# Performance work log

Measured on AMD Instinct MI355X. Metric: run time of the kernel, lower is better.

The kernel has to match this reference:

```python
import jax, jax.numpy as jnp
import numpy as np

NUM_HEADS = 8
LATENT_FRAME = 4
D_MODEL = 1024
D_FF = 1024  # dim_feedforward == output_dim in the torch module
N_LAYERS = 6
IN_DIM = 128
LN_EPS = 1e-5


def get_slopes(n):
    # standard ALiBi slopes for power-of-two head counts: 2^{-8(i+1)/n}
    return jnp.asarray([2.0 ** (-8.0 * (i + 1) / n) for i in range(n)], jnp.float32)


def alibi_mask(num_heads, T):
    # non-causal ('future') ALiBi: additive bias -slope_h * |i - j|, shape (H, T, T)
    dist = jnp.abs(jnp.arange(T)[:, None] - jnp.arange(T)[None, :]).astype(jnp.float32)
    return -get_slopes(num_heads)[:, None, None] * dist


def layernorm(x, g, b):
    m = jnp.mean(x, axis=-1, keepdims=True)
    v = jnp.mean((x - m) ** 2, axis=-1, keepdims=True)
    return (x - m) * jax.lax.rsqrt(v + LN_EPS) * g + b


def encoder_layer(x, p, mask):
    # torch TransformerEncoderLayer, post-norm, gelu(exact), dropout=0
    B, T, D = x.shape
    H, Dh = NUM_HEADS, D // NUM_HEADS
    qkv = x @ p['in_w'].T + p['in_b']                      # (B,T,3D)
    q, k, v = jnp.split(qkv, 3, axis=-1)
    hsplit = lambda t: t.reshape(B, T, H, Dh).transpose(0, 2, 1, 3)  # (B,H,T,Dh)
    q, k, v = hsplit(q), hsplit(k), hsplit(v)
    scores = jnp.einsum('bhqd,bhkd->bhqk', q, k) / float(np.sqrt(Dh)) + mask[None]
    attn = jax.nn.softmax(scores, axis=-1)
    o = jnp.einsum('bhqk,bhkd->bhqd', attn, v).transpose(0, 2, 1, 3).reshape(B, T, D)
    o = o @ p['out_w'].T + p['out_b']
    x = layernorm(x + o, p['ln1_g'], p['ln1_b'])
    ff = jax.nn.gelu(x @ p['ff1_w'].T + p['ff1_b'], approximate=False) @ p['ff2_w'].T + p['ff2_b']
    return layernorm(x + ff, p['ln2_g'], p['ln2_b'])


def setup_inputs() -> dict:
    key = jax.random.key(0)
    ks = iter(jax.random.split(key, 32))
    s = 0.02
    B, T, F = 8, 2048, IN_DIM
    Fs = F * LATENT_FRAME  # 512
    inp = {
        'x': jax.random.normal(next(ks), (B, T, F), jnp.float32),
        'pre_w': jax.random.normal(next(ks), (D_MODEL, Fs), jnp.float32) * s,
        'pre_b': jnp.zeros((D_MODEL,), jnp.float32),
        'in_w': jax.random.normal(next(ks), (N_LAYERS, 3 * D_MODEL, D_MODEL), jnp.float32) * s,
        'in_b': jnp.zeros((N_LAYERS, 3 * D_MODEL), jnp.float32),
        'out_w': jax.random.normal(next(ks), (N_LAYERS, D_MODEL, D_MODEL), jnp.float32) * s,
        'out_b': jnp.zeros((N_LAYERS, D_MODEL), jnp.float32),
        'ln1_g': jnp.ones((N_LAYERS, D_MODEL), jnp.float32),
        'ln1_b': jnp.zeros((N_LAYERS, D_MODEL), jnp.float32),
        'ff1_w': jax.random.normal(next(ks), (N_LAYERS, D_FF, D_MODEL), jnp.float32) * s,
        'ff1_b': jnp.zeros((N_LAYERS, D_FF), jnp.float32),
        'ff2_w': jax.random.normal(next(ks), (N_LAYERS, D_MODEL, D_FF), jnp.float32) * s,
        'ff2_b': jnp.zeros((N_LAYERS, D_MODEL), jnp.float32),
        'ln2_g': jnp.ones((N_LAYERS, D_MODEL), jnp.float32),
        'ln2_b': jnp.zeros((N_LAYERS, D_MODEL), jnp.float32),
        'post_w': jax.random.normal(next(ks), (D_MODEL, D_MODEL), jnp.float32) * s,
        'post_b': jnp.zeros((D_MODEL,), jnp.float32),
    }
    return inp


def reference(x, pre_w, pre_b, in_w, in_b, out_w, out_b, ln1_g, ln1_b,
              ff1_w, ff1_b, ff2_w, ff2_b, ln2_g, ln2_b, post_w, post_b):
    B, T, F = x.shape
    Tl = T // LATENT_FRAME
    x = x.reshape(B, Tl, F * LATENT_FRAME)
    x = x @ pre_w.T + pre_b                     # (B, Tl, D)
    mask = alibi_mask(NUM_HEADS, Tl)            # (H, Tl, Tl), shared by all batches
    layers = dict(in_w=in_w, in_b=in_b, out_w=out_w, out_b=out_b,
                  ln1_g=ln1_g, ln1_b=ln1_b, ff1_w=ff1_w, ff1_b=ff1_b,
                  ff2_w=ff2_w, ff2_b=ff2_b, ln2_g=ln2_g, ln2_b=ln2_b)
    def step(h, p):
        return encoder_layer(h, p, mask), None
    x, _ = jax.lax.scan(step, x, layers)
    return x @ post_w.T + post_b
```

## Files before the change

### kernel.cpp

```cpp
#include <hip/hip_runtime.h>
#include <hip/hip_bf16.h>

#define B 8
#define TL 512
#define M_ROWS 4096
#define D 1024
#define DFF 1024
#define H 8
#define DH 128
#define NL 6

typedef unsigned short ushort_t;
typedef unsigned int uint_t;
typedef short bf16x8 __attribute__((ext_vector_type(8)));
typedef float f32x4 __attribute__((ext_vector_type(4)));

__device__ __forceinline__ ushort_t f2bf(float f) {
    uint_t u = __float_as_uint(f);
    u += 0x7FFFu + ((u >> 16) & 1u);
    return (ushort_t)(u >> 16);
}
__device__ __forceinline__ float gelu_exact(float x) {
    return 0.5f * x * (1.0f + erff(x * 0.70710678118654752f));
}
__device__ __forceinline__ void gload_lds16(const ushort_t* g, ushort_t* l) {
    __builtin_amdgcn_global_load_lds(
        (const __attribute__((address_space(1))) void*)g,
        (__attribute__((address_space(3))) void*)l, 16, 0, 0);
}

struct CvtArgs {
    const float* s[7];
    ushort_t* d[7];
    int nq[7];
    int bstart[8];
};

__global__ __launch_bounds__(256) void cvt_all(CvtArgs a) {
    const int bid = blockIdx.x;
#pragma unroll
    for (int seg = 0; seg < 7; ++seg) {
        const int b0 = a.bstart[seg], b1 = a.bstart[seg + 1];
        if (bid < b0 || bid >= b1) continue;
        const int stride = (b1 - b0) * 256;
        const float* s = a.s[seg];
        ushort_t* d = a.d[seg];
        const int nq = a.nq[seg];
        for (int i = (bid - b0) * 256 + threadIdx.x; i < nq; i += stride) {
            float4 v = *(const float4*)(s + (size_t)i * 4);
            ushort4 o;
            o.x = f2bf(v.x); o.y = f2bf(v.y); o.z = f2bf(v.z); o.w = f2bf(v.w);
            *(ushort4*)(d + (size_t)i * 4) = o;
        }
    }
}

#define LSLOT64(r, c) (((r) * 8 + ((c) ^ ((r) & 7))) * 8)

__global__ __launch_bounds__(512) void gemm_n128(
    const ushort_t* __restrict__ A, const ushort_t* __restrict__ W,
    const float* __restrict__ bias, float* __restrict__ Cf,
    ushort_t* __restrict__ Cb, int M, int N, int K, int do_gelu) {
    extern __shared__ ushort_t lds[];

    const int tid = threadIdx.x;
    const int lane = tid & 63;
    const int w = tid >> 6;
    const int wm = w >> 2;
    const int wn = w & 3;
    const int bm = blockIdx.y * 128;
    const int bn = blockIdx.x * 128;
    const int fr = lane & 15;
    const int fq = lane >> 4;

    const ushort_t* gA[2];
    const ushort_t* gB[2];
    int sdst[2];
#pragma unroll
    for (int u = 0; u < 2; ++u) {
        int s = tid + u * 512;
        int r = s >> 3, c = (s & 7) ^ (r & 7);
        gA[u] = A + (size_t)(bm + r) * K + c * 8;
        gB[u] = W + (size_t)(bn + r) * K + c * 8;
        sdst[u] = s * 8;
    }

    int aoff[4][2], boff[2][2];
#pragma unroll
    for (int ti = 0; ti < 4; ++ti)
#pragma unroll
        for (int ks = 0; ks < 2; ++ks)
            aoff[ti][ks] = LSLOT64(wm * 64 + ti * 16 + fr, ks * 4 + fq);
#pragma unroll
    for (int tj = 0; tj < 2; ++tj)
#pragma unroll
        for (int ks = 0; ks < 2; ++ks)
            boff[tj][ks] = LSLOT64(wn * 32 + tj * 16 + fr, ks * 4 + fq);

    f32x4 acc[4][2];
#pragma unroll
    for (int i = 0; i < 4; ++i)
#pragma unroll
        for (int j = 0; j < 2; ++j) acc[i][j] = (f32x4){0.f, 0.f, 0.f, 0.f};

    auto stage = [&](int buf, int k0) {
#pragma unroll
        for (int u = 0; u < 2; ++u)
            gload_lds16(gA[u] + k0, &lds[buf * 8192 + sdst[u]]);
#pragma unroll
        for (int u = 0; u < 2; ++u)
            gload_lds16(gB[u] + k0, &lds[16384 + buf * 8192 + sdst[u]]);
    };
    auto comp = [&](int buf) {
#pragma unroll
        for (int ks = 0; ks < 2; ++ks) {
            bf16x8 af[4], bfv[2];
#pragma unroll
            for (int ti = 0; ti < 4; ++ti)
                af[ti] = *(const bf16x8*)&lds[buf * 8192 + aoff[ti][ks]];
#pragma unroll
            for (int tj = 0; tj < 2; ++tj)
                bfv[tj] = *(const bf16x8*)&lds[16384 + buf * 8192 + boff[tj][ks]];
#pragma unroll
            for (int i = 0; i < 4; ++i)
#pragma unroll
                for (int j = 0; j < 2; ++j)
                    acc[i][j] = __builtin_amdgcn_mfma_f32_16x16x32_bf16(
                        af[i], bfv[j], acc[i][j], 0, 0, 0);
        }
    };

    const int NT = K >> 6;
    stage(0, 0);
    __syncthreads();
    int buf = 0;
    for (int t = 0; t < NT; ++t) {
        if (t + 1 < NT) stage(buf ^ 1, (t + 1) * 64);
        comp(buf);
        __syncthreads();
        buf ^= 1;
    }

    float bv[2];
#pragma unroll
    for (int tj = 0; tj < 2; ++tj) bv[tj] = bias[bn + wn * 32 + tj * 16 + fr];

    float* eps = (float*)lds;
#pragma unroll
    for (int p = 0; p < 2; ++p) {
        if (p) __syncthreads();
        if (wm == p) {
#pragma unroll
            for (int ti = 0; ti < 4; ++ti)
#pragma unroll
                for (int tj = 0; tj < 2; ++tj)
#pragma unroll
                    for (int r = 0; r < 4; ++r) {
                        float v = acc[ti][tj][r] + bv[tj];
                        if (do_gelu) v = gelu_exact(v);
                        eps[(ti * 16 + fq * 4 + r) * 132 +
                            wn * 32 + tj * 16 + fr] = v;
                    }
        }
        __syncthreads();
#pragma unroll
        for (int k = 0; k < 4; ++k) {
            int f = tid + k * 512;
            int row = f >> 5, c4 = f & 31;
            float4 v = *(const float4*)&eps[row * 132 + c4 * 4];
            const size_t off = (size_t)(bm + p * 64 + row) * N + bn + c4 * 4;
            if (Cf) *(float4*)(Cf + off) = v;
            if (Cb) {
                ushort4 ob;
                ob.x = f2bf(v.x); ob.y = f2bf(v.y);
                ob.z = f2bf(v.z); ob.w = f2bf(v.w);
                *(ushort4*)(Cb + off) = ob;
            }
        }
    }
}

#define QPHASE(par, mh, nh, LOADA, ...)                                        \
    {                                                                          \
        if (LOADA) {                                                           \
            _Pragma("unroll") for (int im = 0; im < 4; ++im)                   \
                _Pragma("unroll") for (int ks = 0; ks < 2; ++ks)               \
                    af[im][ks] = *(const bf16x8*)&AsB[(par)*16384 +            \
                                                     (mh)*8192 + aoff[im][ks]];\
        }                                                                      \
        _Pragma("unroll") for (int jn = 0; jn < 2; ++jn)                       \
            _Pragma("unroll") for (int ks = 0; ks < 2; ++ks)                   \
                bfv[jn][ks] = *(const bf16x8*)&BsB[(par)*16384 +               \
                                                  (nh)*8192 + boff[jn][ks]];   \
        __VA_ARGS__;                                                           \
        __builtin_amdgcn_s_barrier();                                          \
        asm volatile("s_waitcnt lgkmcnt(0)" ::: "memory");                     \
        __builtin_amdgcn_sched_barrier(0);                                     \
        __builtin_amdgcn_s_setprio(1);                                         \
        _Pragma("unroll") for (int im = 0; im < 4; ++im)                       \
            _Pragma("unroll") for (int jn = 0; jn < 2; ++jn)                   \
                _Pragma("unroll") for (int ks = 0; ks < 2; ++ks)               \
                    acc[(mh)*4 + im][(nh)*2 + jn] =                            \
                        __builtin_amdgcn_mfma_f32_16x16x32_bf16(               \
                            af[im][ks], bfv[jn][ks],                           \
                            acc[(mh)*4 + im][(nh)*2 + jn], 0, 0, 0);           \
        __builtin_amdgcn_s_setprio(0);                                         \
        asm volatile("s_waitcnt vmcnt(4)" ::: "memory");                       \
        __builtin_amdgcn_s_barrier();                                          \
    }

__global__ __launch_bounds__(512, 2) void gemm_qkv256(
    const ushort_t* __restrict__ A, const ushort_t* __restrict__ W,
    const float* __restrict__ bias, ushort_t* __restrict__ Qb,
    ushort_t* __restrict__ Kb, ushort_t* __restrict__ Vt) {
    extern __shared__ ushort_t lds[];
    ushort_t* AsB = lds;
    ushort_t* BsB = lds + 32768;
    const int K = 1024;

    const int bid = blockIdx.x;
    const int wg = (bid & 7) * 24 + (bid >> 3);
    const int by = wg / 12, bx = wg - by * 12;
    const int bm = by * 256, bn = bx * 256;

    const int tid = threadIdx.x;
    const int lane = tid & 63;
    const int w = tid >> 6;
    const int wm = w >> 2;
    const int wn = w & 3;
    const int fr = lane & 15;
    const int fq = lane >> 4;

    const ushort_t* gA[2];
    const ushort_t* gB[2];
    int sdst[2];
#pragma unroll
    for (int u = 0; u < 2; ++u) {
        int s = tid + u * 512;
        int r = s >> 3, c = (s & 7) ^ (r & 7);
        gA[u] = A + (size_t)(bm + r) * K + c * 8;
        gB[u] = W + (size_t)(bn + r) * K + c * 8;
        sdst[u] = s * 8;
    }

    int aoff[4][2], boff[2][2];
#pragma unroll
    for (int im = 0; im < 4; ++im)
#pragma unroll
        for (int ks = 0; ks < 2; ++ks)
            aoff[im][ks] = LSLOT64(wm * 64 + im * 16 + fr, ks * 4 + fq);
#pragma unroll
    for (int jn = 0; jn < 2; ++jn)
#pragma unroll
        for (int ks = 0; ks < 2; ++ks)
            boff[jn][ks] = LSLOT64(wn * 32 + jn * 16 + fr, ks * 4 + fq);

    f32x4 acc[8][4];
#pragma unroll
    for (int i = 0; i < 8; ++i)
#pragma unroll
        for (int j = 0; j < 4; ++j) acc[i][j] = (f32x4){0.f, 0.f, 0.f, 0.f};

    auto stageA = [&](int p, int h, int tk) {
#pragma unroll
        for (int u = 0; u < 2; ++u)
            gload_lds16(gA[u] + (size_t)h * 128 * K + tk * 64,
                        &AsB[p * 16384 + h * 8192 + sdst[u]]);
    };
    auto stageB = [&](int p, int h, int tk) {
#pragma unroll
        for (int u = 0; u < 2; ++u)
            gload_lds16(gB[u] + (size_t)h * 128 * K + tk * 64,
                        &BsB[p * 16384 + h * 8192 + sdst[u]]);
    };

    stageA(0, 0, 0); stageB(0, 0, 0); stageB(0, 1, 0); stageA(0, 1, 0);
    asm volatile("s_waitcnt vmcnt(0)" ::: "memory");
    __builtin_amdgcn_s_barrier();

    bf16x8 af[4][2], bfv[2][2];

#pragma unroll 1
    for (int it = 0; it < 8; ++it) {
        const int t0 = 2 * it;
        QPHASE(0, 0, 0, 1, { stageA(1, 0, t0 + 1); })
        QPHASE(0, 0, 1, 0, { stageB(1, 0, t0 + 1); })
        QPHASE(0, 1, 0, 1, { stageB(1, 1, t0 + 1); })
        QPHASE(0, 1, 1, 0, { stageA(1, 1, t0 + 1); })
        const bool st = (it < 7);
        QPHASE(1, 0, 0, 1, { if (st) stageA(0, 0, t0 + 2); })
        QPHASE(1, 0, 1, 0, { if (st) stageB(0, 0, t0 + 2); })
        QPHASE(1, 1, 0, 1, { if (st) stageB(0, 1, t0 + 2); })
        QPHASE(1, 1, 1, 0, { if (st) stageA(0, 1, t0 + 2); })
    }

    const float qscale = 0.08838834764831845f;
#pragma unroll
    for (int j = 0; j < 4; ++j) {
        const int n = bn + (j >> 1) * 128 + wn * 32 + (j & 1) * 16 + fr;
        const float bv = bias[n];
#pragma unroll
        for (int i = 0; i < 8; ++i) {
            const int m0 = bm + (i >> 2) * 128 + wm * 64 + (i & 3) * 16 + fq * 4;
            f32x4 a = acc[i][j];
            if (n < D) {
#pragma unroll
                for (int r = 0; r < 4; ++r)
                    Qb[(size_t)(m0 + r) * D + n] = f2bf((a[r] + bv) * qscale);
            } else if (n < 2 * D) {
#pragma unroll
                for (int r = 0; r < 4; ++r)
                    Kb[(size_t)(m0 + r) * D + (n - D)] = f2bf(a[r] + bv);
            } else {
                const int h = (n - 2 * D) >> 7;
                const int dh = (n - 2 * D) & 127;
                const int bb = m0 >> 9;
                const int t = m0 & 511;
                ushort4 pk;
                pk.x = f2bf(a[0] + bv); pk.y = f2bf(a[1] + bv);
                pk.z = f2bf(a[2] + bv); pk.w = f2bf(a[3] + bv);
                *(ushort4*)&Vt[((size_t)(bb * H + h) * DH + dh) * TL + t] = pk;
            }
        }
    }
}

#define LSW16(r, g) ((((r) << 4) + ((g) ^ ((r) & 7))) << 3)
#define LSW8(r, g) ((((r) << 3) + ((g) ^ ((r) & 7))) << 3)

__global__ __launch_bounds__(256, 2) void attn_mfma(
    const ushort_t* __restrict__ Qb, const ushort_t* __restrict__ Kb,
    const ushort_t* __restrict__ Vt, ushort_t* __restrict__ Ab) {
    __shared__ ushort_t Qs[64 * 128];
    __shared__ ushort_t Ks[64 * 128];
    __shared__ ushort_t Vts[128 * 64];
    __shared__ ushort_t Ps[64 * 72];

    const int q0 = blockIdx.x * 64;
    const int bh = blockIdx.y;
    const int b = bh >> 3;
    const int h = bh & 7;
    const int tid = threadIdx.x;
    const int lane = tid & 63;
    const int w = tid >> 6;
    const int fr = lane & 15;
    const int fq = lane >> 4;

    const float slope = exp2f(-(float)(h + 1));

#pragma unroll
    for (int kk = 0; kk < 4; ++kk) {
        int s = tid + kk * 256;
        int r = s >> 4, gp = s & 15, gl = gp ^ (r & 7);
        gload_lds16(Qb + (size_t)(b * TL + q0 + r) * D + h * DH + gl * 8,
                    &Qs[s * 8]);
    }

    f32x4 o8[8];
    float m_i[4], l_i[4];
#pragma unroll
    for (int nt = 0; nt < 8; ++nt) o8[nt] = (f32x4){0.f, 0.f, 0.f, 0.f};
#pragma unroll
    for (int r = 0; r < 4; ++r) { m_i[r] = -1e30f; l_i[r] = 0.f; }

    for (int kt = 0; kt < TL / 64; ++kt) {
        __syncthreads();
#pragma unroll
        for (int kk = 0; kk < 4; ++kk) {
            int s = tid + kk * 256;
            int r = s >> 4, gp = s & 15, gl = gp ^ (r & 7);
            gload_lds16(Kb + (size_t)(b * TL + kt * 64 + r) * D + h * DH + gl * 8,
                        &Ks[s * 8]);
        }
#pragma unroll
        for (int kk = 0; kk < 4; ++kk) {
            int s = tid + kk * 256;
            int r = s >> 3, gp = s & 7, gl = gp ^ (r & 7);
            gload_lds16(Vt + ((size_t)bh * DH + r) * TL + kt * 64 + gl * 8,
                        &Vts[s * 8]);
        }
        __syncthreads();

        f32x4 sacc[4];
#pragma unroll
        for (int jt = 0; jt < 4; ++jt) sacc[jt] = (f32x4){0.f, 0.f, 0.f, 0.f};
        __builtin_amdgcn_s_setprio(1);
#pragma unroll
        for (int s4 = 0; s4 < 4; ++s4) {
            bf16x8 aq = *(const bf16x8*)&Qs[LSW16(w * 16 + fr, s4 * 4 + fq)];
#pragma unroll
            for (int jt = 0; jt < 4; ++jt) {
                bf16x8 kb = *(const bf16x8*)&Ks[LSW16(jt * 16 + fr, s4 * 4 + fq)];
                sacc[jt] = __builtin_amdgcn_mfma_f32_16x16x32_bf16(
                    aq, kb, sacc[jt], 0, 0, 0);
            }
        }
        __builtin_amdgcn_s_setprio(0);

        const int iq = q0 + w * 16 + fq * 4;
        const int jk = kt * 64 + fr;
        float al[4];
#pragma unroll
        for (int r = 0; r < 4; ++r) {
            float sv[4];
#pragma unroll
            for (int jt = 0; jt < 4; ++jt)
                sv[jt] = sacc[jt][r] -
                         slope * fabsf((float)(iq + r - jk - jt * 16));
            float mx = fmaxf(fmaxf(sv[0], sv[1]), fmaxf(sv[2], sv[3]));
            mx = fmaxf(mx, __shfl_xor(mx, 1));
            mx = fmaxf(mx, __shfl_xor(mx, 2));
            mx = fmaxf(mx, __shfl_xor(mx, 4));
            mx = fmaxf(mx, __shfl_xor(mx, 8));
            float mnew = fmaxf(m_i[r], mx);
            al[r] = __expf(m_i[r] - mnew);
            float rs = 0.f;
#pragma unroll
            for (int jt = 0; jt < 4; ++jt) {
                sv[jt] = __expf(sv[jt] - mnew);
                rs += sv[jt];
            }
            rs += __shfl_xor(rs, 1);
            rs += __shfl_xor(rs, 2);
            rs += __shfl_xor(rs, 4);
            rs += __shfl_xor(rs, 8);
            l_i[r] = l_i[r] * al[r] + rs;
            m_i[r] = mnew;
            const int prow = w * 16 + fq * 4 + r;
#pragma unroll
            for (int jt = 0; jt < 4; ++jt)
                Ps[prow * 72 + jt * 16 + fr] = f2bf(sv[jt]);
        }
#pragma unroll
        for (int nt = 0; nt < 8; ++nt)
#pragma unroll
            for (int r = 0; r < 4; ++r) o8[nt][r] *= al[r];

        __builtin_amdgcn_s_setprio(1);
#pragma unroll
        for (int s2 = 0; s2 < 2; ++s2) {
            bf16x8 pa = *(const bf16x8*)&Ps[(w * 16 + fr) * 72 + s2 * 32 + fq * 8];
#pragma unroll
            for (int nt = 0; nt < 8; ++nt) {
                bf16x8 vb = *(const bf16x8*)&Vts[LSW8(nt * 16 + fr, s2 * 4 + fq)];
                o8[nt] = __builtin_amdgcn_mfma_f32_16x16x32_bf16(
                    pa, vb, o8[nt], 0, 0, 0);
            }
        }
        __builtin_amdgcn_s_setprio(0);
    }

#pragma unroll
    for (int r = 0; r < 4; ++r) {
        float inv = 1.f / l_i[r];
        const size_t base = (size_t)(b * TL + q0 + w * 16 + fq * 4 + r) * D + h * DH;
#pragma unroll
        for (int nt = 0; nt < 8; ++nt)
            Ab[base + nt * 16 + fr] = f2bf(o8[nt][r] * inv);
    }
}

__global__ __launch_bounds__(256) void add_ln(const float* __restrict__ x,
                                              const float* __restrict__ y,
                                              const float* __restrict__ g,
                                              const float* __restrict__ bta,
                                              float* __restrict__ out,
                                              ushort_t* __restrict__ outb) {
    const int row = blockIdx.x * 4 + (threadIdx.x >> 6);
    const int lane = threadIdx.x & 63;
    const size_t rbase = (size_t)row * D;

    float4 v[4];
#pragma unroll
    for (int j = 0; j < 4; ++j) {
        float4 xv = *(const float4*)(x + rbase + lane * 4 + j * 256);
        float4 yv = *(const float4*)(y + rbase + lane * 4 + j * 256);
        v[j].x = xv.x + yv.x; v[j].y = xv.y + yv.y;
        v[j].z = xv.z + yv.z; v[j].w = xv.w + yv.w;
    }

    float s = 0.f;
#pragma unroll
    for (int j = 0; j < 4; ++j) s += v[j].x + v[j].y + v[j].z + v[j].w;
#pragma unroll
    for (int off = 32; off; off >>= 1) s += __shfl_xor(s, off);
    const float mean = s * (1.f / (float)D);

    float sq = 0.f;
#pragma unroll
    for (int j = 0; j < 4; ++j) {
        float d0 = v[j].x - mean, d1 = v[j].y - mean;
        float d2 = v[j].z - mean, d3 = v[j].w - mean;
        sq += d0 * d0 + d1 * d1 + d2 * d2 + d3 * d3;
    }
#pragma unroll
    for (int off = 32; off; off >>= 1) sq += __shfl_xor(sq, off);
    const float var = sq * (1.f / (float)D);
    const float inv = rsqrtf(var + 1e-5f);

#pragma unroll
    for (int j = 0; j < 4; ++j) {
        const int col = lane * 4 + j * 256;
        float4 gv = *(const float4*)(g + col);
        float4 bv = *(const float4*)(bta + col);
        float4 o;
        o.x = (v[j].x - mean) * inv * gv.x + bv.x;
        o.y = (v[j].y - mean) * inv * gv.y + bv.y;
        o.z = (v[j].z - mean) * inv * gv.z + bv.z;
        o.w = (v[j].w - mean) * inv * gv.w + bv.w;
        *(float4*)(out + rbase + col) = o;
        ushort4 ob;
        ob.x = f2bf(o.x); ob.y = f2bf(o.y); ob.z = f2bf(o.z); ob.w = f2bf(o.w);
        *(ushort4*)(outb + rbase + col) = ob;
    }
}

extern "C" void kernel_launch(void* const* d_in, const int* in_sizes, int n_in,
                              void* d_out, int out_size, void* d_ws, size_t ws_size,
                              hipStream_t stream) {
    const float* x_in   = (const float*)d_in[0];
    const float* pre_w  = (const float*)d_in[1];
    const float* pre_b  = (const float*)d_in[2];
    const float* in_w   = (const float*)d_in[3];
    const float* in_b   = (const float*)d_in[4];
    const float* out_w  = (const float*)d_in[5];
    const float* out_b  = (const float*)d_in[6];
    const float* ln1_g  = (const float*)d_in[7];
    const float* ln1_b  = (const float*)d_in[8];
    const float* ff1_w  = (const float*)d_in[9];
    const float* ff1_b  = (const float*)d_in[10];
    const float* ff2_w  = (const float*)d_in[11];
    const float* ff2_b  = (const float*)d_in[12];
    const float* ln2_g  = (const float*)d_in[13];
    const float* ln2_b  = (const float*)d_in[14];
    const float* post_w = (const float*)d_in[15];
    const float* post_b = (const float*)d_in[16];

    static bool attr_set = false;
    if (!attr_set) {
        hipFuncSetAttribute((const void*)gemm_qkv256,
                            hipFuncAttributeMaxDynamicSharedMemorySize, 131072);
        hipFuncSetAttribute((const void*)gemm_n128,
                            hipFuncAttributeMaxDynamicSharedMemorySize, 65536);
        attr_set = true;
    }

    float* X = (float*)d_ws;
    float* Y = X + (size_t)M_ROWS * D;
    ushort_t* Xb   = (ushort_t*)(Y + (size_t)M_ROWS * D);
    ushort_t* Ab   = Xb + (size_t)M_ROWS * D;
    ushort_t* Qb   = Ab + (size_t)M_ROWS * D;
    ushort_t* Kb   = Qb + (size_t)M_ROWS * D;
    ushort_t* Vt   = Kb + (size_t)M_ROWS * D;
    ushort_t* xinb = Vt + (size_t)M_ROWS * D;
    ushort_t* pwb  = xinb + (size_t)M_ROWS * 512;
    ushort_t* iwb  = pwb + (size_t)D * 512;
    ushort_t* owb  = iwb + (size_t)NL * 3 * D * D;
    ushort_t* f1wb = owb + (size_t)NL * D * D;
    ushort_t* f2wb = f1wb + (size_t)NL * DFF * D;
    ushort_t* powb = f2wb + (size_t)NL * D * DFF;

    const dim3 blk(256);

    CvtArgs ca;
    ca.s[0] = x_in;   ca.d[0] = xinb; ca.nq[0] = (M_ROWS * 512) / 4;
    ca.s[1] = pre_w;  ca.d[1] = pwb;  ca.nq[1] = (D * 512) / 4;
    ca.s[2] = in_w;   ca.d[2] = iwb;  ca.nq[2] = (NL * 3 * D * D) / 4;
    ca.s[3] = out_w;  ca.d[3] = owb;  ca.nq[3] = (NL * D * D) / 4;
    ca.s[4] = ff1_w;  ca.d[4] = f1wb; ca.nq[4] = (NL * DFF * D) / 4;
    ca.s[5] = ff2_w;  ca.d[5] = f2wb; ca.nq[5] = (NL * D * DFF) / 4;
    ca.s[6] = post_w; ca.d[6] = powb; ca.nq[6] = (D * D) / 4;
    {
        long long total = 0;
        for (int i = 0; i < 7; ++i) total += ca.nq[i];
        long long cum = 0;
        ca.bstart[0] = 0;
        for (int i = 0; i < 7; ++i) {
            cum += ca.nq[i];
            ca.bstart[i + 1] = (int)((cum * 4096) / total);
        }
        ca.bstart[7] = 4096;
    }
    cvt_all<<<4096, blk, 0, stream>>>(ca);

    const dim3 gN128(D / 128, M_ROWS / 128);

    gemm_n128<<<gN128, dim3(512), 65536, stream>>>(xinb, pwb, pre_b, X, Xb,
                                                   M_ROWS, D, 512, 0);

    for (int l = 0; l < NL; ++l) {
        gemm_qkv256<<<dim3(192), dim3(512), 131072, stream>>>(
            Xb, iwb + (size_t)l * 3 * D * D, in_b + (size_t)l * 3 * D,
            Qb, Kb, Vt);
        attn_mfma<<<dim3(TL / 64, B * H), blk, 0, stream>>>(Qb, Kb, Vt, Ab);
        gemm_n128<<<gN128, dim3(512), 65536, stream>>>(
            Ab, owb + (size_t)l * D * D, out_b + (size_t)l * D, Y, nullptr,
            M_ROWS, D, D, 0);
        add_ln<<<dim3(M_ROWS / 4), blk, 0, stream>>>(X, Y, ln1_g + (size_t)l * D,
                                                     ln1_b + (size_t)l * D, X, Xb);
        gemm_n128<<<gN128, dim3(512), 65536, stream>>>(
            Xb, f1wb + (size_t)l * DFF * D, ff1_b + (size_t)l * DFF, nullptr, Ab,
            M_ROWS, DFF, D, 1);
        gemm_n128<<<gN128, dim3(512), 65536, stream>>>(
            Ab, f2wb + (size_t)l * D * DFF, ff2_b + (size_t)l * D, Y, nullptr,
            M_ROWS, D, DFF, 0);
        add_ln<<<dim3(M_ROWS / 4), blk, 0, stream>>>(X, Y, ln2_g + (size_t)l * D,
                                                     ln2_b + (size_t)l * D, X, Xb);
    }

    gemm_n128<<<gN128, dim3(512), 65536, stream>>>(Xb, powb, post_b,
                                                   (float*)d_out, nullptr,
                                                   M_ROWS, D, D, 0);
}
```

Baseline: 1.127 ms.

## Use triple-buffered K pipeline in GEMMs and replace 256-tile QKV kernel with 128-tile

Replaces the double-buffered K loop in gemm_n128 with a three-stage LDS ring buffer that keeps two tiles in flight, using vmcnt waits and one barrier per step, and raises MFMA priority during compute. The hand-scheduled 256x256 QKV GEMM is swapped for a 128x128 variant that uses the same pipeline, with 768 blocks instead of 192, and stages Q/K output through LDS for coalesced stores. The intent is to hide global load latency and improve occupancy and load balance. In exchange it uses more LDS per block (96KB), which may cut blocks per CU, and it loses the 256-tile data reuse in QKV.

```diff
diff --git a/kernel.cpp b/kernel.cpp
--- a/kernel.cpp
+++ b/kernel.cpp
@@ -57,6 +57,26 @@
 
 #define LSLOT64(r, c) (((r) * 8 + ((c) ^ ((r) & 7))) * 8)
 
+#define PIPE_K_LOOP(NT)                                                        \
+    {                                                                          \
+        stage(0, 0);                                                           \
+        stage(1, 64);                                                          \
+        int bsel = 0;                                                          \
+        for (int t = 0; t < (NT)-1; ++t) {                                     \
+            asm volatile("s_waitcnt vmcnt(4)" ::: "memory");                   \
+            __builtin_amdgcn_s_barrier();                                      \
+            comp(bsel);                                                        \
+            if (t + 2 < (NT)) {                                                \
+                int nb = bsel + 2; if (nb >= 3) nb -= 3;                       \
+                stage(nb, (t + 2) * 64);                                       \
+            }                                                                  \
+            ++bsel; if (bsel == 3) bsel = 0;                                   \
+        }                                                                      \
+        asm volatile("s_waitcnt vmcnt(0)" ::: "memory");                       \
+        __builtin_amdgcn_s_barrier();                                          \
+        comp(bsel);                                                            \
+    }
+
 __global__ __launch_bounds__(512) void gemm_n128(
     const ushort_t* __restrict__ A, const ushort_t* __restrict__ W,
     const float* __restrict__ bias, float* __restrict__ Cf,
@@ -106,10 +126,10 @@
     auto stage = [&](int buf, int k0) {
 #pragma unroll
         for (int u = 0; u < 2; ++u)
-            gload_lds16(gA[u] + k0, &lds[buf * 8192 + sdst[u]]);
+            gload_lds16(gA[u] + k0, &lds[buf * 16384 + sdst[u]]);
 #pragma unroll
         for (int u = 0; u < 2; ++u)
-            gload_lds16(gB[u] + k0, &lds[16384 + buf * 8192 + sdst[u]]);
+            gload_lds16(gB[u] + k0, &lds[buf * 16384 + 8192 + sdst[u]]);
     };
     auto comp = [&](int buf) {
 #pragma unroll
@@ -117,29 +137,24 @@
             bf16x8 af[4], bfv[2];
 #pragma unroll
             for (int ti = 0; ti < 4; ++ti)
-                af[ti] = *(const bf16x8*)&lds[buf * 8192 + aoff[ti][ks]];
+                af[ti] = *(const bf16x8*)&lds[buf * 16384 + aoff[ti][ks]];
 #pragma unroll
             for (int tj = 0; tj < 2; ++tj)
-                bfv[tj] = *(const bf16x8*)&lds[16384 + buf * 8192 + boff[tj][ks]];
+                bfv[tj] = *(const bf16x8*)&lds[buf * 16384 + 8192 + boff[tj][ks]];
+            __builtin_amdgcn_s_setprio(1);
 #pragma unroll
             for (int i = 0; i < 4; ++i)
 #pragma unroll
                 for (int j = 0; j < 2; ++j)
                     acc[i][j] = __builtin_amdgcn_mfma_f32_16x16x32_bf16(
                         af[i], bfv[j], acc[i][j], 0, 0, 0);
+            __builtin_amdgcn_s_setprio(0);
         }
     };
 
     const int NT = K >> 6;
-    stage(0, 0);
+    PIPE_K_LOOP(NT)
     __syncthreads();
-    int buf = 0;
-    for (int t = 0; t < NT; ++t) {
-        if (t + 1 < NT) stage(buf ^ 1, (t + 1) * 64);
-        comp(buf);
-        __syncthreads();
-        buf ^= 1;
-    }
 
     float bv[2];
 #pragma unroll
@@ -180,48 +195,17 @@
     }
 }
 
-#define QPHASE(par, mh, nh, LOADA, ...)                                        \
-    {                                                                          \
-        if (LOADA) {                                                           \
-            _Pragma("unroll") for (int im = 0; im < 4; ++im)                   \
-                _Pragma("unroll") for (int ks = 0; ks < 2; ++ks)               \
-                    af[im][ks] = *(const bf16x8*)&AsB[(par)*16384 +            \
-                                                     (mh)*8192 + aoff[im][ks]];\
-        }                                                                      \
-        _Pragma("unroll") for (int jn = 0; jn < 2; ++jn)                       \
-            _Pragma("unroll") for (int ks = 0; ks < 2; ++ks)                   \
-                bfv[jn][ks] = *(const bf16x8*)&BsB[(par)*16384 +               \
-                                                  (nh)*8192 + boff[jn][ks]];   \
-        __VA_ARGS__;                                                           \
-        __builtin_amdgcn_s_barrier();                                          \
-        asm volatile("s_waitcnt lgkmcnt(0)" ::: "memory");                     \
-        __builtin_amdgcn_sched_barrier(0);                                     \
-        __builtin_amdgcn_s_setprio(1);                                         \
-        _Pragma("unroll") for (int im = 0; im < 4; ++im)                       \
-            _Pragma("unroll") for (int jn = 0; jn < 2; ++jn)                   \
-                _Pragma("unroll") for (int ks = 0; ks < 2; ++ks)               \
-                    acc[(mh)*4 + im][(nh)*2 + jn] =                            \
-                        __builtin_amdgcn_mfma_f32_16x16x32_bf16(               \
-                            af[im][ks], bfv[jn][ks],                           \
-                            acc[(mh)*4 + im][(nh)*2 + jn], 0, 0, 0);           \
-        __builtin_amdgcn_s_setprio(0);                                         \
-        asm volatile("s_waitcnt vmcnt(4)" ::: "memory");                       \
-        __builtin_amdgcn_s_barrier();                                          \
-    }
-
-__global__ __launch_bounds__(512, 2) void gemm_qkv256(
+__global__ __launch_bounds__(512) void gemm_qkv128(
     const ushort_t* __restrict__ A, const ushort_t* __restrict__ W,
     const float* __restrict__ bias, ushort_t* __restrict__ Qb,
     ushort_t* __restrict__ Kb, ushort_t* __restrict__ Vt) {
     extern __shared__ ushort_t lds[];
-    ushort_t* AsB = lds;
-    ushort_t* BsB = lds + 32768;
     const int K = 1024;
 
     const int bid = blockIdx.x;
-    const int wg = (bid & 7) * 24 + (bid >> 3);
-    const int by = wg / 12, bx = wg - by * 12;
-    const int bm = by * 256, bn = bx * 256;
+    const int wg = (bid & 7) * 96 + (bid >> 3);
+    const int by = wg / 24, bx = wg - by * 24;
+    const int bm = by * 128, bn = bx * 128;
 
     const int tid = threadIdx.x;
     const int lane = tid & 63;
@@ -245,80 +229,106 @@
 
     int aoff[4][2], boff[2][2];
 #pragma unroll
-    for (int im = 0; im < 4; ++im)
+    for (int ti = 0; ti < 4; ++ti)
 #pragma unroll
         for (int ks = 0; ks < 2; ++ks)
-            aoff[im][ks] = LSLOT64(wm * 64 + im * 16 + fr, ks * 4 + fq);
-#pragma unroll
-    for (int jn = 0; jn < 2; ++jn)
+            aoff[ti][ks] = LSLOT64(wm * 64 + ti * 16 + fr, ks * 4 + fq);
+#pragma unroll
+    for (int tj = 0; tj < 2; ++tj)
 #pragma unroll
         for (int ks = 0; ks < 2; ++ks)
-            boff[jn][ks] = LSLOT64(wn * 32 + jn * 16 + fr, ks * 4 + fq);
-
-    f32x4 acc[8][4];
-#pragma unroll
-    for (int i = 0; i < 8; ++i)
-#pragma unroll
-        for (int j = 0; j < 4; ++j) acc[i][j] = (f32x4){0.f, 0.f, 0.f, 0.f};
-
-    auto stageA = [&](int p, int h, int tk) {
+            boff[tj][ks] = LSLOT64(wn * 32 + tj * 16 + fr, ks * 4 + fq);
+
+    f32x4 acc[4][2];
+#pragma unroll
+    for (int i = 0; i < 4; ++i)
+#pragma unroll
+        for (int j = 0; j < 2; ++j) acc[i][j] = (f32x4){0.f, 0.f, 0.f, 0.f};
+
+    auto stage = [&](int buf, int k0) {
 #pragma unroll
         for (int u = 0; u < 2; ++u)
-            gload_lds16(gA[u] + (size_t)h * 128 * K + tk * 64,
-                        &AsB[p * 16384 + h * 8192 + sdst[u]]);
+            gload_lds16(gA[u] + k0, &lds[buf * 16384 + sdst[u]]);
+#pragma unroll
+        for (int u = 0; u < 2; ++u)
+            gload_lds16(gB[u] + k0, &lds[buf * 16384 + 8192 + sdst[u]]);
     };
-    auto stageB = [&](int p, int h, int tk) {
-#pragma unroll
-        for (int u = 0; u < 2; ++u)
-            gload_lds16(gB[u] + (size_t)h * 128 * K + tk * 64,
-                        &BsB[p * 16384 + h * 8192 + sdst[u]]);
+    auto comp = [&](int buf) {
+#pragma unroll
+        for (int ks = 0; ks < 2; ++ks) {
+            bf16x8 af[4], bfv[2];
+#pragma unroll
+            for (int ti = 0; ti < 4; ++ti)
+                af[ti] = *(const bf16x8*)&lds[buf * 16384 + aoff[ti][ks]];
+#pragma unroll
+            for (int tj = 0; tj < 2; ++tj)
+                bfv[tj] = *(const bf16x8*)&lds[buf * 16384 + 8192 + boff[tj][ks]];
+            __builtin_amdgcn_s_setprio(1);
+#pragma unroll
+            for (int i = 0; i < 4; ++i)
+#pragma unroll
+                for (int j = 0; j < 2; ++j)
+                    acc[i][j] = __builtin_amdgcn_mfma_f32_16x16x32_bf16(
+                        af[i], bfv[j], acc[i][j], 0, 0, 0);
+            __builtin_amdgcn_s_setprio(0);
+        }
     };
 
-    stageA(0, 0, 0); stageB(0, 0, 0); stageB(0, 1, 0); stageA(0, 1, 0);
-    asm volatile("s_waitcnt vmcnt(0)" ::: "memory");
-    __builtin_amdgcn_s_barrier();
-
-    bf16x8 af[4][2], bfv[2][2];
-
-#pragma unroll 1
-    for (int it = 0; it < 8; ++it) {
-        const int t0 = 2 * it;
-        QPHASE(0, 0, 0, 1, { stageA(1, 0, t0 + 1); })
-        QPHASE(0, 0, 1, 0, { stageB(1, 0, t0 + 1); })
-        QPHASE(0, 1, 0, 1, { stageB(1, 1, t0 + 1); })
-        QPHASE(0, 1, 1, 0, { stageA(1, 1, t0 + 1); })
-        const bool st = (it < 7);
-        QPHASE(1, 0, 0, 1, { if (st) stageA(0, 0, t0 + 2); })
-        QPHASE(1, 0, 1, 0, { if (st) stageB(0, 0, t0 + 2); })
-        QPHASE(1, 1, 0, 1, { if (st) stageB(0, 1, t0 + 2); })
-        QPHASE(1, 1, 1, 0, { if (st) stageA(0, 1, t0 + 2); })
-    }
+    PIPE_K_LOOP(16)
 
     const float qscale = 0.08838834764831845f;
-#pragma unroll
-    for (int j = 0; j < 4; ++j) {
-        const int n = bn + (j >> 1) * 128 + wn * 32 + (j & 1) * 16 + fr;
-        const float bv = bias[n];
-#pragma unroll
-        for (int i = 0; i < 8; ++i) {
-            const int m0 = bm + (i >> 2) * 128 + wm * 64 + (i & 3) * 16 + fq * 4;
-            f32x4 a = acc[i][j];
-            if (n < D) {
-#pragma unroll
-                for (int r = 0; r < 4; ++r)
-                    Qb[(size_t)(m0 + r) * D + n] = f2bf((a[r] + bv) * qscale);
-            } else if (n < 2 * D) {
-#pragma unroll
-                for (int r = 0; r < 4; ++r)
-                    Kb[(size_t)(m0 + r) * D + (n - D)] = f2bf(a[r] + bv);
-            } else {
-                const int h = (n - 2 * D) >> 7;
-                const int dh = (n - 2 * D) & 127;
+    float bv[2];
+#pragma unroll
+    for (int tj = 0; tj < 2; ++tj) bv[tj] = bias[bn + wn * 32 + tj * 16 + fr];
+
+    if (bn < 2 * D) {
+        __syncthreads();
+        const float scale = (bn < D) ? qscale : 1.f;
+        ushort_t* dst = (bn < D) ? Qb : Kb;
+        const int nc0 = (bn < D) ? bn : bn - D;
+        float* eps = (float*)lds;
+#pragma unroll
+        for (int p = 0; p < 2; ++p) {
+            if (p) __syncthreads();
+            if (wm == p) {
+#pragma unroll
+                for (int ti = 0; ti < 4; ++ti)
+#pragma unroll
+                    for (int tj = 0; tj < 2; ++tj)
+#pragma unroll
+                        for (int r = 0; r < 4; ++r)
+                            eps[(ti * 16 + fq * 4 + r) * 132 +
+                                wn * 32 + tj * 16 + fr] =
+                                (acc[ti][tj][r] + bv[tj]) * scale;
+            }
+            __syncthreads();
+#pragma unroll
+            for (int k = 0; k < 4; ++k) {
+                int f = tid + k * 512;
+                int row = f >> 5, c4 = f & 31;
+                float4 v = *(const float4*)&eps[row * 132 + c4 * 4];
+                ushort4 ob;
+                ob.x = f2bf(v.x); ob.y = f2bf(v.y);
+                ob.z = f2bf(v.z); ob.w = f2bf(v.w);
+                *(ushort4*)(dst + (size_t)(bm + p * 64 + row) * D + nc0 +
+                            c4 * 4) = ob;
+            }
+        }
+    } else {
+#pragma unroll
+        for (int tj = 0; tj < 2; ++tj) {
+            const int n = bn + wn * 32 + tj * 16 + fr;
+            const int h = (n - 2 * D) >> 7;
+            const int dh = (n - 2 * D) & 127;
+#pragma unroll
+            for (int ti = 0; ti < 4; ++ti) {
+                const int m0 = bm + wm * 64 + ti * 16 + fq * 4;
                 const int bb = m0 >> 9;
                 const int t = m0 & 511;
+                f32x4 a = acc[ti][tj];
                 ushort4 pk;
-                pk.x = f2bf(a[0] + bv); pk.y = f2bf(a[1] + bv);
-                pk.z = f2bf(a[2] + bv); pk.w = f2bf(a[3] + bv);
+                pk.x = f2bf(a[0] + bv[tj]); pk.y = f2bf(a[1] + bv[tj]);
+                pk.z = f2bf(a[2] + bv[tj]); pk.w = f2bf(a[3] + bv[tj]);
                 *(ushort4*)&Vt[((size_t)(bb * H + h) * DH + dh) * TL + t] = pk;
             }
         }
@@ -538,10 +548,10 @@
 
     static bool attr_set = false;
     if (!attr_set) {
-        hipFuncSetAttribute((const void*)gemm_qkv256,
-                            hipFuncAttributeMaxDynamicSharedMemorySize, 131072);
         hipFuncSetAttribute((const void*)gemm_n128,
-                            hipFuncAttributeMaxDynamicSharedMemorySize, 65536);
+                            hipFuncAttributeMaxDynamicSharedMemorySize, 98304);
+        hipFuncSetAttribute((const void*)gemm_qkv128,
+                            hipFuncAttributeMaxDynamicSharedMemorySize, 98304);
         attr_set = true;
     }
 
@@ -585,30 +595,30 @@
 
     const dim3 gN128(D / 128, M_ROWS / 128);
 
-    gemm_n128<<<gN128, dim3(512), 65536, stream>>>(xinb, pwb, pre_b, X, Xb,
+    gemm_n128<<<gN128, dim3(512), 98304, stream>>>(xinb, pwb, pre_b, X, Xb,
                                                    M_ROWS, D, 512, 0);
 
     for (int l = 0; l < NL; ++l) {
-        gemm_qkv256<<<dim3(192), dim3(512), 131072, stream>>>(
+        gemm_qkv128<<<dim3(768), dim3(512), 98304, stream>>>(
             Xb, iwb + (size_t)l * 3 * D * D, in_b + (size_t)l * 3 * D,
             Qb, Kb, Vt);
         attn_mfma<<<dim3(TL / 64, B * H), blk, 0, stream>>>(Qb, Kb, Vt, Ab);
-        gemm_n128<<<gN128, dim3(512), 65536, stream>>>(
+        gemm_n128<<<gN128, dim3(512), 98304, stream>>>(
             Ab, owb + (size_t)l * D * D, out_b + (size_t)l * D, Y, nullptr,
             M_ROWS, D, D, 0);
         add_ln<<<dim3(M_ROWS / 4), blk, 0, stream>>>(X, Y, ln1_g + (size_t)l * D,
                                                      ln1_b + (size_t)l * D, X, Xb);
-        gemm_n128<<<gN128, dim3(512), 65536, stream>>>(
+        gemm_n128<<<gN128, dim3(512), 98304, stream>>>(
             Xb, f1wb + (size_t)l * DFF * D, ff1_b + (size_t)l * DFF, nullptr, Ab,
             M_ROWS, DFF, D, 1);
-        gemm_n128<<<gN128, dim3(512), 65536, stream>>>(
+        gemm_n128<<<gN128, dim3(512), 98304, stream>>>(
             Ab, f2wb + (size_t)l * D * DFF, ff2_b + (size_t)l * D, Y, nullptr,
             M_ROWS, D, DFF, 0);
         add_ln<<<dim3(M_ROWS / 4), blk, 0, stream>>>(X, Y, ln2_g + (size_t)l * D,
                                                      ln2_b + (size_t)l * D, X, Xb);
     }
 
-    gemm_n128<<<gN128, dim3(512), 65536, stream>>>(Xb, powb, post_b,
+    gemm_n128<<<gN128, dim3(512), 98304, stream>>>(Xb, powb, post_b,
                                                    (float*)d_out, nullptr,
                                                    M_ROWS, D, D, 0);
 }
```

Result: faster. 1.082 ms, median of 2 (-4.0%).
